# Kernel tuning notes

Hardware: AMD Instinct MI355X
Metric: run time of the kernel (lower is better)

The kernel has to match this reference:

```python
import jax, jax.numpy as jnp
import numpy as np

jax.config.update("jax_enable_x64", True)

C = 62          # in/conv channels
T = 2000        # time samples
B = 256         # batch
VEC_DIM = C * (C + 1) // 2  # 1953
HIDDEN = 64
NUM_CLASSES = 3
SPD_EPS = 1e-3
LOGMAP_EPS = 1e-6


def setup_inputs() -> dict:
    key = jax.random.key(0)
    ks = jax.random.split(key, 8)
    x = jax.random.normal(ks[0], (B, C, T), dtype=jnp.float32)
    # Conv1d kernel_size=1 == per-timestep channel mixing: weight [out_c, in_c]
    conv_w = jax.random.normal(ks[1], (C, C), dtype=jnp.float32) / np.sqrt(C)
    conv_b = jax.random.normal(ks[2], (C,), dtype=jnp.float32) * 0.01
    proj_w = jax.random.normal(ks[3], (HIDDEN, VEC_DIM), dtype=jnp.float32) / np.sqrt(VEC_DIM)
    proj_b = jax.random.normal(ks[4], (HIDDEN,), dtype=jnp.float32) * 0.01
    head_w = jax.random.normal(ks[5], (NUM_CLASSES, HIDDEN), dtype=jnp.float32) / np.sqrt(HIDDEN)
    head_b = jax.random.normal(ks[6], (NUM_CLASSES,), dtype=jnp.float32) * 0.01
    return {"x": x, "conv_w": conv_w, "conv_b": conv_b,
            "proj_w": proj_w, "proj_b": proj_b,
            "head_w": head_w, "head_b": head_b}


def _forward(x, conv_w, conv_b, proj_w, proj_b, head_w, head_b):
    # Conv1d with kernel_size=1: [B,C,T] -> [B,C,T]
    xc = jnp.einsum('oc,bct->bot', conv_w, x) + conv_b[None, :, None]
    # covariance in double precision (torch code does .double())
    xc64 = xc.astype(jnp.float64)
    x_cen = xc64 - xc64.mean(axis=2, keepdims=True)
    denom = float(max(1, T - 1))
    cov = jnp.einsum('bct,bdt->bcd', x_cen, x_cen) / denom  # [B,C,C]
    cov = 0.5 * (cov + jnp.swapaxes(cov, 1, 2))
    # SPD regularization + re-symmetrize
    cov = cov + SPD_EPS * jnp.eye(C, dtype=jnp.float64)
    cov = 0.5 * (cov + jnp.swapaxes(cov, 1, 2))
    # log-map: eigh, clamp, log, reconstruct
    vals, vecs = jnp.linalg.eigh(cov)                       # [B,C], [B,C,C]
    log_vals = jnp.log(jnp.maximum(vals, LOGMAP_EPS))
    log_cov = jnp.einsum('bik,bk,bjk->bij', vecs, log_vals, vecs)
    # upper-triangular (incl. diag) vectorization, row-major like torch.triu_indices
    iu, ju = jnp.triu_indices(C)
    vec = log_cov[:, iu, ju].astype(jnp.float32)            # [B, 1953]
    feat = jax.nn.relu(vec @ proj_w.T + proj_b)             # [B, 64]
    logits = feat @ head_w.T + head_b                       # [B, 3]
    return logits


def reference(x, conv_w, conv_b, proj_w, proj_b, head_w, head_b):
    return _forward(x, conv_w, conv_b, proj_w, proj_b, head_w, head_b)
```

## Files before the change

### kernel.cpp

```cpp
#include <hip/hip_runtime.h>
#include <math.h>

#define CC 62
#define TT 2000
#define BB 256
#define VECN 1953
#define HID 64
#define NCLS 3
#define NG 31
#define LDX 68
#define XBUF (64 * LDX)
#define NT1 32
#define SLD 64
#define LDGF 68

typedef const unsigned int __attribute__((address_space(1)))* gbl_u32p;
typedef unsigned int __attribute__((address_space(3)))* lds_u32p;

#define WAITV(n) asm volatile("s_waitcnt vmcnt(" #n ")" ::: "memory")

__device__ __forceinline__ void decodePi(int pi, int& i, int& j)
{
    int ii = 0, rem = pi;
    while (rem >= CC - ii) { rem -= (CC - ii); ++ii; }
    i = ii; j = ii + rem;
}

__device__ __forceinline__ void pairPQ(int r, int k, int& p, int& q)
{
    if (k == 0) { p = 0; q = 1 + (r + 60) % 61; }
    else {
        p = 1 + (r + k - 1) % 61;
        q = 1 + (r + 60 - k) % 61;
    }
    if (p > q) { int t = p; p = q; q = t; }
}

__global__ __launch_bounds__(576) void fused(
    const float* __restrict__ x, const float* __restrict__ cw,
    const float* __restrict__ pw, const float* __restrict__ pbias,
    const float* __restrict__ hw, const float* __restrict__ hb,
    float* __restrict__ out)
{
    const int b = blockIdx.x, tid = threadIdx.x;
    const int wid = tid >> 6, lane = tid & 63;

    __shared__ __align__(16) double sA[4352];
    __shared__ __align__(16) double sC[VECN];
    __shared__ double sU[9 * 64];
    __shared__ double sNorm[64];
    __shared__ double sD[64];
    __shared__ double sMean[64];
    __shared__ unsigned short sPair[61 * NG];
    __shared__ int    sFlag;
    __shared__ float  sF[HID];

    float*  sX   = reinterpret_cast<float*>(sA);
    double* sS   = sA;
    float*  sGf  = reinterpret_cast<float*>(sA);
    float*  sVec = reinterpret_cast<float*>(sC);

    const int slot = tid >> 2, myks = tid & 3;
    const bool actA = (slot < 136);
    int gi = 0, gj = 0;
    if (actA) {
        int g = 0, rem = slot;
        while (rem >= 16 - g) { rem -= (16 - g); ++g; }
        gi = g; gj = g + rem;
    }
    const int a0 = 4 * gi, b0 = 4 * gj;
    const int pA = gi >> 1, pB = gj >> 1;

    double acc[4][4];
    float  accf[4][4];
#pragma unroll
    for (int r = 0; r < 4; ++r)
#pragma unroll
        for (int c = 0; c < 4; ++c) { acc[r][c] = 0.0; accf[r][c] = 0.0f; }

    for (int e = tid; e < 61 * NG; e += 576) {
        int r = e / NG, k = e - r * NG;
        int p, q; pairPQ(r, k, p, q);
        sPair[e] = (unsigned short)(p | (q << 8));
    }
    if (tid < 128) {
        int bu = tid >> 6, t = tid & 63;
        sX[bu * XBUF + 62 * LDX + t] = 1.0f;
        sX[bu * XBUF + 63 * LDX + t] = 0.0f;
    }
    __syncthreads();

    const float* xb = x + (size_t)b * (CC * TT);

    auto issueTile = [&](int buf, int tile) {
        const int t0 = tile * 64;
        for (int c = wid; c < CC; c += 9) {
            const int ps = c >> 3;
            const int tt = 4 * ((lane >> 2) ^ ps) + (lane & 3);
            if (t0 + tt < TT) {
                const float* gp = xb + (size_t)c * TT + t0 + tt;
                __builtin_amdgcn_global_load_lds(
                    (gbl_u32p)gp, (lds_u32p)&sX[buf * XBUF + c * LDX], 4, 0, 0);
            }
        }
    };

    issueTile(0, 0);
    for (int tile = 0; tile < NT1; ++tile) {
        const int cur = tile & 1;
        __builtin_amdgcn_s_barrier();
        if (tile + 1 < NT1) {
            issueTile(cur ^ 1, tile + 1);
            if (wid < 8) WAITV(7); else WAITV(6);
        } else {
            WAITV(0);
        }
        __builtin_amdgcn_sched_barrier(0);
        __builtin_amdgcn_s_barrier();
        if (actA) {
            const float* xt = &sX[cur * XBUF];
            const int nq = min(16, (TT - tile * 64) >> 2);
            for (int m = myks; m < nq; m += 4) {
                const int ca = 4 * (m ^ pA), cb = 4 * (m ^ pB);
                float4 af[4], bf[4];
#pragma unroll
                for (int r = 0; r < 4; ++r)
                    af[r] = *reinterpret_cast<const float4*>(&xt[(a0 + r) * LDX + ca]);
#pragma unroll
                for (int r = 0; r < 4; ++r)
                    bf[r] = *reinterpret_cast<const float4*>(&xt[(b0 + r) * LDX + cb]);
#pragma unroll
                for (int k = 0; k < 4; ++k) {
#pragma unroll
                    for (int r = 0; r < 4; ++r)
#pragma unroll
                        for (int s = 0; s < 4; ++s)
                            accf[r][s] += (&af[r].x)[k] * (&bf[s].x)[k];
                }
            }
#pragma unroll
            for (int r = 0; r < 4; ++r)
#pragma unroll
                for (int c = 0; c < 4; ++c) {
                    acc[r][c] += (double)accf[r][c];
                    accf[r][c] = 0.0f;
                }
        }
    }

#pragma unroll
    for (int r = 0; r < 4; ++r)
#pragma unroll
        for (int c = 0; c < 4; ++c) {
            double v = acc[r][c];
            v += __shfl_xor(v, 1, 4);
            v += __shfl_xor(v, 2, 4);
            acc[r][c] = v;
        }
    __syncthreads();
    if (actA && myks == 0) {
#pragma unroll
        for (int r = 0; r < 4; ++r)
#pragma unroll
            for (int c = 0; c < 4; ++c)
                sS[(a0 + r) * SLD + (b0 + c)] = acc[r][c];
    }
    __syncthreads();

    if (tid < CC) sMean[tid] = sS[tid * SLD + 62] / (double)TT;
    __syncthreads();

    for (int pi = tid; pi < VECN; pi += 576) {
        int i, j; decodePi(pi, i, j);
        sC[pi] = (sS[i * SLD + j] - (double)TT * sMean[i] * sMean[j]) / 1999.0;
    }
    __syncthreads();

    for (int e = tid; e < CC * LDGF; e += 576) sGf[e] = 0.0f;
    __syncthreads();

    const int jj = tid >> 6, kk = tid & 63;
    for (int j0 = 0; j0 < CC; j0 += 9) {
        const int j = j0 + jj;
        if (kk < CC && j < CC) {
            const float* wr = cw + j * CC;
            double a = 0.0; int idx = kk;
            for (int l = 0; l < kk; ++l) { a += sC[idx] * (double)wr[l]; idx += 61 - l; }
            for (int l = kk; l < CC; ++l) { a += sC[idx] * (double)wr[l]; idx += 1; }
            sU[jj * 64 + kk] = a;
        }
        __syncthreads();
        const int i = kk;
        if (i < CC && j < CC && i <= j) {
            const float* wi = cw + i * CC;
            double a = (i == j) ? 1e-3 : 0.0;
            for (int l = 0; l < CC; ++l) a += (double)wi[l] * sU[jj * 64 + l];
            sGf[j * LDGF + i] = (float)a;
            sGf[i * LDGF + j] = (float)a;
        }
        __syncthreads();
    }

    if (tid < CC) {
        const float* col = &sGf[tid * LDGF];
        double n = 0.0;
        for (int i2 = 0; i2 < CC; ++i2) n += (double)col[i2] * (double)col[i2];
        sNorm[tid] = n;
    }
    __syncthreads();

    const int g = tid >> 4, lt = tid & 15;
    const bool actJ = (g < NG);
    const int r0 = 4 * lt;

    for (int sweep = 0; sweep < 20; ++sweep) {
        if (tid == 0) sFlag = 0;
        __syncthreads();
        for (int r = 0; r < 61; ++r) {
            if (actJ) {
                int pq = sPair[r * NG + g];
                int p = pq & 255, q = pq >> 8;
                float4* gp = reinterpret_cast<float4*>(&sGf[p * LDGF + r0]);
                float4* gq = reinterpret_cast<float4*>(&sGf[q * LDGF + r0]);
                float4 P = *gp, Q = *gq;
                float df = P.x * Q.x + P.y * Q.y + P.z * Q.z + P.w * Q.w;
                { int t2 = __builtin_amdgcn_mov_dpp(__float_as_int(df), 0xB1, 0xF, 0xF, true);
                  df += __int_as_float(t2); }
                { int t2 = __builtin_amdgcn_mov_dpp(__float_as_int(df), 0x4E, 0xF, 0xF, true);
                  df += __int_as_float(t2); }
                { int t2 = __builtin_amdgcn_mov_dpp(__float_as_int(df), 0x141, 0xF, 0xF, true);
                  df += __int_as_float(t2); }
                { int t2 = __builtin_amdgcn_mov_dpp(__float_as_int(df), 0x140, 0xF, 0xF, true);
                  df += __int_as_float(t2); }
                double d = (double)df;
                double np = sNorm[p], nq = sNorm[q];
                double d2 = d * d, bb = np * nq;
                if (d2 > bb * 1e-12) {
                    float npf = (float)np, nqf = (float)nq;
                    float thf = (nqf - npf) *
                                __builtin_amdgcn_rcpf(2.0f * df);
                    float a2 = fabsf(thf);
                    float tf = __builtin_amdgcn_rcpf(
                        a2 + __builtin_amdgcn_sqrtf(fmaf(a2, a2, 1.0f)));
                    if (thf < 0.0f) tf = -tf;
                    float cf = __builtin_amdgcn_rsqf(fmaf(tf, tf, 1.0f));
                    float sn = tf * cf;
                    *gp = make_float4(cf * P.x - sn * Q.x, cf * P.y - sn * Q.y,
                                      cf * P.z - sn * Q.z, cf * P.w - sn * Q.w);
                    *gq = make_float4(sn * P.x + cf * Q.x, sn * P.y + cf * Q.y,
                                      sn * P.z + cf * Q.z, sn * P.w + cf * Q.w);
                    if (lt == 0) {
                        double td = (double)tf * d;
                        sNorm[p] = np - td; sNorm[q] = nq + td;
                        if (d2 > bb * 1e-9) sFlag = 1;
                    }
                }
            }
            __syncthreads();
        }
        int flag = sFlag;
        __syncthreads();
        if (!flag) break;
    }

    if (tid < CC) {
        const float* col = &sGf[tid * LDGF];
        double n = 0.0;
        for (int i5 = 0; i5 < CC; ++i5) n += (double)col[i5] * (double)col[i5];
        double lamv = sqrt(n);
        sD[tid] = log(fmax(lamv, 1e-6)) / n;
    }
    __syncthreads();

    for (int pi = tid; pi < VECN; pi += 576) {
        int i, j; decodePi(pi, i, j);
        double a = 0.0;
        for (int k2 = 0; k2 < CC; ++k2)
            a += sD[k2] * (double)sGf[k2 * LDGF + i] * (double)sGf[k2 * LDGF + j];
        sVec[pi] = (float)a;
    }
    __syncthreads();

    if (wid < 8) {
        for (int hh = 0; hh < 8; ++hh) {
            const int h = wid * 8 + hh;
            const float* w = pw + (size_t)h * VECN;
            float a = 0.0f;
            for (int k = lane; k < VECN; k += 64) a += sVec[k] * w[k];
            a += __shfl_xor(a, 32); a += __shfl_xor(a, 16); a += __shfl_xor(a, 8);
            a += __shfl_xor(a, 4);  a += __shfl_xor(a, 2);  a += __shfl_xor(a, 1);
            if (lane == 0) sF[h] = fmaxf(a + pbias[h], 0.0f);
        }
    }
    __syncthreads();
    if (tid < NCLS) {
        float o = hb[tid];
        for (int hh = 0; hh < HID; ++hh) o += sF[hh] * hw[tid * HID + hh];
        out[b * NCLS + tid] = o;
    }
}

extern "C" void kernel_launch(void* const* d_in, const int* in_sizes, int n_in,
                              void* d_out, int out_size, void* d_ws, size_t ws_size,
                              hipStream_t stream)
{
    const float* x  = (const float*)d_in[0];
    const float* cw = (const float*)d_in[1];
    const float* pw = (const float*)d_in[3];
    const float* pb = (const float*)d_in[4];
    const float* hw = (const float*)d_in[5];
    const float* hb = (const float*)d_in[6];
    float* out = (float*)d_out;

    fused<<<BB, 576, 0, stream>>>(x, cw, pw, pb, hw, hb, out);
}
```

Baseline: 634.0 us.

## Run one-sided Jacobi in registers of a single wavefront with shuffles

The Jacobi eigen-sweep moves out of LDS with block-wide barriers per round and into a single wavefront. Each lane holds one 64-float column in registers and fetches its partner column via __shfl, so the per-round __syncthreads and the sPair table are gone. The block shrinks from 576 to 512 threads, and the covariance k-split changes from 4 to 2. The cost is that 64 shuffles per rotation and heavy register pressure fall on one wave while the other seven idle during the eigen phase.

```diff
diff --git a/kernel.cpp b/kernel.cpp
--- a/kernel.cpp
+++ b/kernel.cpp
@@ -7,7 +7,6 @@
 #define VECN 1953
 #define HID 64
 #define NCLS 3
-#define NG 31
 #define LDX 68
 #define XBUF (64 * LDX)
 #define NT1 32
@@ -26,17 +25,7 @@
     i = ii; j = ii + rem;
 }
 
-__device__ __forceinline__ void pairPQ(int r, int k, int& p, int& q)
-{
-    if (k == 0) { p = 0; q = 1 + (r + 60) % 61; }
-    else {
-        p = 1 + (r + k - 1) % 61;
-        q = 1 + (r + 60 - k) % 61;
-    }
-    if (p > q) { int t = p; p = q; q = t; }
-}
-
-__global__ __launch_bounds__(576) void fused(
+__global__ __launch_bounds__(512) void fused(
     const float* __restrict__ x, const float* __restrict__ cw,
     const float* __restrict__ pw, const float* __restrict__ pbias,
     const float* __restrict__ hw, const float* __restrict__ hb,
@@ -47,12 +36,9 @@
 
     __shared__ __align__(16) double sA[4352];
     __shared__ __align__(16) double sC[VECN];
-    __shared__ double sU[9 * 64];
-    __shared__ double sNorm[64];
+    __shared__ double sU[8 * 64];
     __shared__ double sD[64];
     __shared__ double sMean[64];
-    __shared__ unsigned short sPair[61 * NG];
-    __shared__ int    sFlag;
     __shared__ float  sF[HID];
 
     float*  sX   = reinterpret_cast<float*>(sA);
@@ -60,13 +46,13 @@
     float*  sGf  = reinterpret_cast<float*>(sA);
     float*  sVec = reinterpret_cast<float*>(sC);
 
-    const int slot = tid >> 2, myks = tid & 3;
+    const int slot = tid >> 1, ksA = tid & 1;
     const bool actA = (slot < 136);
     int gi = 0, gj = 0;
     if (actA) {
-        int g = 0, rem = slot;
-        while (rem >= 16 - g) { rem -= (16 - g); ++g; }
-        gi = g; gj = g + rem;
+        int g2 = 0, rem = slot;
+        while (rem >= 16 - g2) { rem -= (16 - g2); ++g2; }
+        gi = g2; gj = g2 + rem;
     }
     const int a0 = 4 * gi, b0 = 4 * gj;
     const int pA = gi >> 1, pB = gj >> 1;
@@ -78,11 +64,6 @@
 #pragma unroll
         for (int c = 0; c < 4; ++c) { acc[r][c] = 0.0; accf[r][c] = 0.0f; }
 
-    for (int e = tid; e < 61 * NG; e += 576) {
-        int r = e / NG, k = e - r * NG;
-        int p, q; pairPQ(r, k, p, q);
-        sPair[e] = (unsigned short)(p | (q << 8));
-    }
     if (tid < 128) {
         int bu = tid >> 6, t = tid & 63;
         sX[bu * XBUF + 62 * LDX + t] = 1.0f;
@@ -94,7 +75,7 @@
 
     auto issueTile = [&](int buf, int tile) {
         const int t0 = tile * 64;
-        for (int c = wid; c < CC; c += 9) {
+        for (int c = wid; c < CC; c += 8) {
             const int ps = c >> 3;
             const int tt = 4 * ((lane >> 2) ^ ps) + (lane & 3);
             if (t0 + tt < TT) {
@@ -111,7 +92,7 @@
         __builtin_amdgcn_s_barrier();
         if (tile + 1 < NT1) {
             issueTile(cur ^ 1, tile + 1);
-            if (wid < 8) WAITV(7); else WAITV(6);
+            if (wid < 6) WAITV(8); else WAITV(7);
         } else {
             WAITV(0);
         }
@@ -119,8 +100,8 @@
         __builtin_amdgcn_s_barrier();
         if (actA) {
             const float* xt = &sX[cur * XBUF];
-            const int nq = min(16, (TT - tile * 64) >> 2);
-            for (int m = myks; m < nq; m += 4) {
+            const int nqm = min(16, (TT - tile * 64) >> 2);
+            for (int m = ksA; m < nqm; m += 2) {
                 const int ca = 4 * (m ^ pA), cb = 4 * (m ^ pB);
                 float4 af[4], bf[4];
 #pragma unroll
@@ -151,14 +132,10 @@
 #pragma unroll
     for (int r = 0; r < 4; ++r)
 #pragma unroll
-        for (int c = 0; c < 4; ++c) {
-            double v = acc[r][c];
-            v += __shfl_xor(v, 1, 4);
-            v += __shfl_xor(v, 2, 4);
-            acc[r][c] = v;
-        }
-    __syncthreads();
-    if (actA && myks == 0) {
+        for (int c = 0; c < 4; ++c)
+            acc[r][c] += __shfl_xor(acc[r][c], 1, 2);
+    __syncthreads();
+    if (actA && ksA == 0) {
 #pragma unroll
         for (int r = 0; r < 4; ++r)
 #pragma unroll
@@ -170,17 +147,17 @@
     if (tid < CC) sMean[tid] = sS[tid * SLD + 62] / (double)TT;
     __syncthreads();
 
-    for (int pi = tid; pi < VECN; pi += 576) {
+    for (int pi = tid; pi < VECN; pi += 512) {
         int i, j; decodePi(pi, i, j);
         sC[pi] = (sS[i * SLD + j] - (double)TT * sMean[i] * sMean[j]) / 1999.0;
     }
     __syncthreads();
 
-    for (int e = tid; e < CC * LDGF; e += 576) sGf[e] = 0.0f;
+    for (int e = tid; e < CC * LDGF; e += 512) sGf[e] = 0.0f;
     __syncthreads();
 
     const int jj = tid >> 6, kk = tid & 63;
-    for (int j0 = 0; j0 < CC; j0 += 9) {
+    for (int j0 = 0; j0 < CC; j0 += 8) {
         const int j = j0 + jj;
         if (kk < CC && j < CC) {
             const float* wr = cw + j * CC;
@@ -201,78 +178,76 @@
         __syncthreads();
     }
 
-    if (tid < CC) {
-        const float* col = &sGf[tid * LDGF];
+    if (wid == 0 && lane < CC) {
+        float g[64], pv[64];
+#pragma unroll
+        for (int k = 0; k < 16; ++k) {
+            float4 v = *reinterpret_cast<const float4*>(&sGf[lane * LDGF + 4 * k]);
+            g[4 * k] = v.x; g[4 * k + 1] = v.y; g[4 * k + 2] = v.z; g[4 * k + 3] = v.w;
+        }
         double n = 0.0;
-        for (int i2 = 0; i2 < CC; ++i2) n += (double)col[i2] * (double)col[i2];
-        sNorm[tid] = n;
-    }
-    __syncthreads();
-
-    const int g = tid >> 4, lt = tid & 15;
-    const bool actJ = (g < NG);
-    const int r0 = 4 * lt;
-
-    for (int sweep = 0; sweep < 20; ++sweep) {
-        if (tid == 0) sFlag = 0;
-        __syncthreads();
-        for (int r = 0; r < 61; ++r) {
-            if (actJ) {
-                int pq = sPair[r * NG + g];
-                int p = pq & 255, q = pq >> 8;
-                float4* gp = reinterpret_cast<float4*>(&sGf[p * LDGF + r0]);
-                float4* gq = reinterpret_cast<float4*>(&sGf[q * LDGF + r0]);
-                float4 P = *gp, Q = *gq;
-                float df = P.x * Q.x + P.y * Q.y + P.z * Q.z + P.w * Q.w;
-                { int t2 = __builtin_amdgcn_mov_dpp(__float_as_int(df), 0xB1, 0xF, 0xF, true);
-                  df += __int_as_float(t2); }
-                { int t2 = __builtin_amdgcn_mov_dpp(__float_as_int(df), 0x4E, 0xF, 0xF, true);
-                  df += __int_as_float(t2); }
-                { int t2 = __builtin_amdgcn_mov_dpp(__float_as_int(df), 0x141, 0xF, 0xF, true);
-                  df += __int_as_float(t2); }
-                { int t2 = __builtin_amdgcn_mov_dpp(__float_as_int(df), 0x140, 0xF, 0xF, true);
-                  df += __int_as_float(t2); }
-                double d = (double)df;
-                double np = sNorm[p], nq = sNorm[q];
-                double d2 = d * d, bb = np * nq;
+#pragma unroll
+        for (int k = 0; k < 64; ++k) n = fma((double)g[k], (double)g[k], n);
+
+        for (int sweep = 0; sweep < 20; ++sweep) {
+            int flagAny = 0;
+            for (int r = 0; r < 61; ++r) {
+                int partner;
+                if (lane == 0) partner = 1 + (r + 60) % 61;
+                else {
+                    int a2 = (lane - 1 - r + 61) % 61;
+                    partner = (a2 == 60) ? 0 : 1 + (r + 59 - a2) % 61;
+                }
+                const bool isP = lane < partner;
+#pragma unroll
+                for (int k = 0; k < 64; ++k) pv[k] = __shfl(g[k], partner);
+                float d0 = 0.f, d1 = 0.f, d2f = 0.f, d3 = 0.f;
+#pragma unroll
+                for (int k = 0; k < 64; k += 4) {
+                    d0 = fmaf(g[k],     pv[k],     d0);
+                    d1 = fmaf(g[k + 1], pv[k + 1], d1);
+                    d2f = fmaf(g[k + 2], pv[k + 2], d2f);
+                    d3 = fmaf(g[k + 3], pv[k + 3], d3);
+                }
+                float df = (d0 + d1) + (d2f + d3);
+                double npart = __shfl(n, partner);
+                double np = isP ? n : npart, nq2 = isP ? npart : n;
+                double dd = (double)df, d2 = dd * dd, bb = np * nq2;
                 if (d2 > bb * 1e-12) {
-                    float npf = (float)np, nqf = (float)nq;
-                    float thf = (nqf - npf) *
-                                __builtin_amdgcn_rcpf(2.0f * df);
-                    float a2 = fabsf(thf);
+                    float npf = (float)np, nqf = (float)nq2;
+                    float thf = (nqf - npf) * __builtin_amdgcn_rcpf(2.0f * df);
+                    float a3 = fabsf(thf);
                     float tf = __builtin_amdgcn_rcpf(
-                        a2 + __builtin_amdgcn_sqrtf(fmaf(a2, a2, 1.0f)));
+                        a3 + __builtin_amdgcn_sqrtf(fmaf(a3, a3, 1.0f)));
                     if (thf < 0.0f) tf = -tf;
                     float cf = __builtin_amdgcn_rsqf(fmaf(tf, tf, 1.0f));
                     float sn = tf * cf;
-                    *gp = make_float4(cf * P.x - sn * Q.x, cf * P.y - sn * Q.y,
-                                      cf * P.z - sn * Q.z, cf * P.w - sn * Q.w);
-                    *gq = make_float4(sn * P.x + cf * Q.x, sn * P.y + cf * Q.y,
-                                      sn * P.z + cf * Q.z, sn * P.w + cf * Q.w);
-                    if (lt == 0) {
-                        double td = (double)tf * d;
-                        sNorm[p] = np - td; sNorm[q] = nq + td;
-                        if (d2 > bb * 1e-9) sFlag = 1;
-                    }
+                    float ss = isP ? -sn : sn;
+#pragma unroll
+                    for (int k = 0; k < 64; ++k)
+                        g[k] = fmaf(cf, g[k], ss * pv[k]);
+                    double td = (double)tf * dd;
+                    n += isP ? -td : td;
+                    if (d2 > bb * 1e-9) flagAny = 1;
                 }
             }
-            __syncthreads();
-        }
-        int flag = sFlag;
-        __syncthreads();
-        if (!flag) break;
-    }
-
-    if (tid < CC) {
-        const float* col = &sGf[tid * LDGF];
-        double n = 0.0;
-        for (int i5 = 0; i5 < CC; ++i5) n += (double)col[i5] * (double)col[i5];
-        double lamv = sqrt(n);
-        sD[tid] = log(fmax(lamv, 1e-6)) / n;
-    }
-    __syncthreads();
-
-    for (int pi = tid; pi < VECN; pi += 576) {
+            if (!__any(flagAny)) break;
+        }
+
+#pragma unroll
+        for (int k = 0; k < 16; ++k) {
+            float4 v = make_float4(g[4 * k], g[4 * k + 1], g[4 * k + 2], g[4 * k + 3]);
+            *reinterpret_cast<float4*>(&sGf[lane * LDGF + 4 * k]) = v;
+        }
+        double nf = 0.0;
+#pragma unroll
+        for (int k = 0; k < 64; ++k) nf = fma((double)g[k], (double)g[k], nf);
+        double lamv = sqrt(nf);
+        sD[lane] = log(fmax(lamv, 1e-6)) / nf;
+    }
+    __syncthreads();
+
+    for (int pi = tid; pi < VECN; pi += 512) {
         int i, j; decodePi(pi, i, j);
         double a = 0.0;
         for (int k2 = 0; k2 < CC; ++k2)
@@ -281,7 +256,7 @@
     }
     __syncthreads();
 
-    if (wid < 8) {
+    {
         for (int hh = 0; hh < 8; ++hh) {
             const int h = wid * 8 + hh;
             const float* w = pw + (size_t)h * VECN;
@@ -312,5 +287,5 @@
     const float* hb = (const float*)d_in[6];
     float* out = (float*)d_out;
 
-    fused<<<BB, 576, 0, stream>>>(x, cw, pw, pb, hw, hb, out);
+    fused<<<BB, 512, 0, stream>>>(x, cw, pw, pb, hw, hb, out);
 }
```

Result: slower. 855.1 us (+34.9%).
